# Performance work log

Hardware: AMD Instinct MI355X
Metric: run time of the kernel (lower is better)

Reference implementation:

```python
import jax, jax.numpy as jnp
import numpy as np

B, S, D, H = 2, 2048, 512, 8
HD = D // H
DFF = 4 * D
EPS_LN = 1e-5
EPS_ATTN = 1e-8


def layernorm(x, w, b):
    mu = jnp.mean(x, axis=-1, keepdims=True)
    var = jnp.var(x, axis=-1, keepdims=True)
    return (x - mu) * jax.lax.rsqrt(var + EPS_LN) * w + b


def masked_attention(q_src, v_src, wq, bq, wk, bk, wv, bv, wo, bo, M):
    # q_src/v_src: (B,S,D); M: (B,S,S)
    Bs, Ss, _ = q_src.shape
    Q = (q_src @ wq + bq).reshape(Bs, Ss, H, HD)
    K = (q_src @ wk + bk).reshape(Bs, Ss, H, HD)
    V = (v_src @ wv + bv).reshape(Bs, Ss, H, HD)
    scale = HD ** -0.5
    scores = jnp.einsum('bqhd,bkhd->bhqk', Q, K) * scale
    Mh = M[:, None, :, :]                      # (B,1,S,S) broadcast over heads
    scores = scores * Mh
    A = jax.nn.softmax(scores, axis=-1)
    A = A * Mh                                 # re-mask post-softmax
    A = A / (jnp.sum(jnp.abs(A), axis=-1, keepdims=True) + EPS_ATTN)  # L1 renorm
    out = jnp.einsum('bhqk,bkhd->bqhd', A, V).reshape(Bs, Ss, D)
    return out @ wo + bo


def ffn(x, w1, b1, w2, b2):
    h = jax.nn.gelu(x @ w1 + b1, approximate=False)
    return x + (h @ w2 + b2)                   # FeedForward(num_layers=2) includes residual


def setup_inputs() -> dict:
    key = jax.random.key(0)
    ks = iter(jax.random.split(key, 64))
    nrm = lambda shape, s=0.02: jax.random.normal(next(ks), shape, jnp.float32) * s
    d = {
        'gene_emb': jax.random.normal(next(ks), (B, S, D), jnp.float32),
        'expr_emb': jax.random.normal(next(ks), (B, S, D), jnp.float32),
        'M': jax.random.uniform(next(ks), (B, S, S), jnp.float32),
    }
    # gene attention params (weights stored (in,out))
    for p in ['g_wq', 'g_wk', 'g_wv', 'g_wo']:
        d[p] = nrm((D, D))
    for p in ['g_bq', 'g_bk', 'g_bv', 'g_bo']:
        d[p] = jnp.zeros((D,), jnp.float32)
    # expr attention params (fused proj 2D->D)
    d['e_wf'] = nrm((2 * D, D)); d['e_bf'] = jnp.zeros((D,), jnp.float32)
    for p in ['e_wq', 'e_wk', 'e_wv', 'e_wo']:
        d[p] = nrm((D, D))
    for p in ['e_bq', 'e_bk', 'e_bv', 'e_bo']:
        d[p] = jnp.zeros((D,), jnp.float32)
    # layernorms
    for p in ['ln_g1_w', 'ln_g2_w', 'ln_e1_w', 'ln_e2_w']:
        d[p] = jnp.ones((D,), jnp.float32)
    for p in ['ln_g1_b', 'ln_g2_b', 'ln_e1_b', 'ln_e2_b']:
        d[p] = jnp.zeros((D,), jnp.float32)
    # FFNs
    d['fg_w1'] = nrm((D, DFF)); d['fg_b1'] = jnp.zeros((DFF,), jnp.float32)
    d['fg_w2'] = nrm((DFF, D)); d['fg_b2'] = jnp.zeros((D,), jnp.float32)
    d['fe_w1'] = nrm((D, DFF)); d['fe_b1'] = jnp.zeros((DFF,), jnp.float32)
    d['fe_w2'] = nrm((DFF, D)); d['fe_b2'] = jnp.zeros((D,), jnp.float32)
    return d


def reference(gene_emb, expr_emb, M,
              g_wq, g_bq, g_wk, g_bk, g_wv, g_bv, g_wo, g_bo,
              e_wf, e_bf, e_wq, e_bq, e_wk, e_bk, e_wv, e_bv, e_wo, e_bo,
              ln_g1_w, ln_g1_b, ln_g2_w, ln_g2_b,
              ln_e1_w, ln_e1_b, ln_e2_w, ln_e2_b,
              fg_w1, fg_b1, fg_w2, fg_b2,
              fe_w1, fe_b1, fe_w2, fe_b2):
    # ----- gene branch -----
    xg = layernorm(gene_emb, ln_g1_w, ln_g1_b)
    attn_g = masked_attention(xg, xg, g_wq, g_bq, g_wk, g_bk, g_wv, g_bv, g_wo, g_bo, M)
    x = gene_emb + attn_g
    x_ln = layernorm(x, ln_g2_w, ln_g2_b)
    out_gene = x + ffn(x_ln, fg_w1, fg_b1, fg_w2, fg_b2)
    # ----- expression branch -----
    y_n = layernorm(expr_emb, ln_e1_w, ln_e1_b)
    fused = jnp.concatenate([gene_emb, y_n], axis=-1) @ e_wf + e_bf
    attn_e = masked_attention(fused, y_n, e_wq, e_bq, e_wk, e_bk, e_wv, e_bv, e_wo, e_bo, M)
    y = expr_emb + attn_e
    y_ln = layernorm(y, ln_e2_w, ln_e2_b)
    out_expr = y + ffn(y_ln, fe_w1, fe_b1, fe_w2, fe_b2)
    return (out_gene, out_expr)
```

## Files before the change

### kernel.cpp

```cpp
#include <hip/hip_runtime.h>
#include <math.h>

#define S_LEN 2048
#define DMODEL 512
#define NROWS 4096
#define NHEAD 8
#define HDIM 64
#define LOG2E 1.4426950408889634f

typedef __attribute__((ext_vector_type(8))) __bf16 bf16x8;
typedef __attribute__((ext_vector_type(4))) float f32x4;

__device__ inline float bf2f(unsigned short h) {
    unsigned u = ((unsigned)h) << 16;
    return __builtin_bit_cast(float, u);
}
__device__ inline unsigned short f2bf(float f) {
    unsigned u = __builtin_bit_cast(unsigned, f);
    return (unsigned short)((u + 0x7fffu + ((u >> 16) & 1u)) >> 16);
}

__device__ inline void gl_lds16(const unsigned short* g, unsigned short* l) {
    __builtin_amdgcn_global_load_lds(
        (const __attribute__((address_space(1))) void*)g,
        (__attribute__((address_space(3))) void*)l, 16, 0, 0);
}

__global__ __launch_bounds__(256) void wcast_t(
    const float* __restrict__ W, unsigned short* __restrict__ Wt, int K, int Mo)
{
    __shared__ float t[32][33];
    const int bx = blockIdx.x * 32;
    const int by = blockIdx.y * 32;
    const int tx = threadIdx.x & 31, ty = threadIdx.x >> 5;
    #pragma unroll
    for (int r = 0; r < 4; ++r)
        t[ty + 8 * r][tx] = W[(size_t)(by + ty + 8 * r) * Mo + bx + tx];
    __syncthreads();
    #pragma unroll
    for (int r = 0; r < 4; ++r)
        Wt[(size_t)(bx + ty + 8 * r) * K + by + tx] = f2bf(t[tx][ty + 8 * r]);
}

__global__ __launch_bounds__(256) void wcast_sq8(
    const float* w0, const float* w1, const float* w2, const float* w3,
    const float* w4, const float* w5, const float* w6, const float* w7,
    unsigned short* __restrict__ dst)
{
    const float* srcs[8] = {w0, w1, w2, w3, w4, w5, w6, w7};
    const float* __restrict__ W = srcs[blockIdx.z];
    unsigned short* __restrict__ Wt = dst + (size_t)blockIdx.z * 512 * 512;
    __shared__ float t[32][33];
    const int bx = blockIdx.x * 32, by = blockIdx.y * 32;
    const int tx = threadIdx.x & 31, ty = threadIdx.x >> 5;
    #pragma unroll
    for (int r = 0; r < 4; ++r)
        t[ty + 8 * r][tx] = W[(size_t)(by + ty + 8 * r) * 512 + bx + tx];
    __syncthreads();
    #pragma unroll
    for (int r = 0; r < 4; ++r)
        Wt[(size_t)(bx + ty + 8 * r) * 512 + by + tx] = f2bf(t[tx][ty + 8 * r]);
}

__global__ __launch_bounds__(256) void wcast_t2(
    const float* wA, const float* wB, unsigned short* __restrict__ dst,
    int K, int Mo)
{
    const float* __restrict__ W = blockIdx.z ? wB : wA;
    unsigned short* __restrict__ Wt = dst + (size_t)blockIdx.z * K * Mo;
    __shared__ float t[32][33];
    const int bx = blockIdx.x * 32, by = blockIdx.y * 32;
    const int tx = threadIdx.x & 31, ty = threadIdx.x >> 5;
    #pragma unroll
    for (int r = 0; r < 4; ++r)
        t[ty + 8 * r][tx] = W[(size_t)(by + ty + 8 * r) * Mo + bx + tx];
    __syncthreads();
    #pragma unroll
    for (int r = 0; r < 4; ++r)
        Wt[(size_t)(bx + ty + 8 * r) * K + by + tx] = f2bf(t[tx][ty + 8 * r]);
}

__global__ __launch_bounds__(256) void pack_bias(
    const float* __restrict__ b1, const float* __restrict__ b2,
    const float* __restrict__ b3, float* __restrict__ dst, int n)
{
    int t = blockIdx.x * 256 + threadIdx.x;
    if (t >= n) return;
    float v = (t < 512) ? b1[t] : (t < 1024) ? b2[t - 512] : b3[t - 1024];
    dst[t] = v;
}

__global__ __launch_bounds__(256) void ln_kernel(
    const float* __restrict__ x, const float* __restrict__ w,
    const float* __restrict__ b, unsigned short* __restrict__ y, int ostride)
{
    __shared__ float red[8];
    const int row = blockIdx.x;
    const float* xr = x + (size_t)row * DMODEL;
    const int t = threadIdx.x;
    float v0 = xr[t];
    float v1 = xr[t + 256];
    float s  = v0 + v1;
    float sq = v0 * v0 + v1 * v1;
    #pragma unroll
    for (int o = 32; o > 0; o >>= 1) {
        s  += __shfl_down(s, o);
        sq += __shfl_down(sq, o);
    }
    int wid = t >> 6, lane = t & 63;
    if (lane == 0) { red[wid] = s; red[4 + wid] = sq; }
    __syncthreads();
    float mean = (red[0] + red[1] + red[2] + red[3]) * (1.0f / 512.0f);
    float msq  = (red[4] + red[5] + red[6] + red[7]) * (1.0f / 512.0f);
    float var  = msq - mean * mean;
    float rs   = rsqrtf(var + 1e-5f);
    y[(size_t)row * ostride + t]       = f2bf((v0 - mean) * rs * w[t] + b[t]);
    y[(size_t)row * ostride + t + 256] = f2bf((v1 - mean) * rs * w[t + 256] + b[t + 256]);
}

__global__ __launch_bounds__(256) void ln_cat_kernel(
    const float* __restrict__ xg, const float* __restrict__ xe,
    const float* __restrict__ w, const float* __restrict__ b,
    unsigned short* __restrict__ y)
{
    __shared__ float red[8];
    const int row = blockIdx.x;
    const int t = threadIdx.x;
    const float* gr = xg + (size_t)row * DMODEL;
    const float* er = xe + (size_t)row * DMODEL;
    float g0 = gr[t], g1 = gr[t + 256];
    float v0 = er[t], v1 = er[t + 256];
    float s  = v0 + v1;
    float sq = v0 * v0 + v1 * v1;
    #pragma unroll
    for (int o = 32; o > 0; o >>= 1) {
        s  += __shfl_down(s, o);
        sq += __shfl_down(sq, o);
    }
    int wid = t >> 6, lane = t & 63;
    if (lane == 0) { red[wid] = s; red[4 + wid] = sq; }
    __syncthreads();
    float mean = (red[0] + red[1] + red[2] + red[3]) * (1.0f / 512.0f);
    float msq  = (red[4] + red[5] + red[6] + red[7]) * (1.0f / 512.0f);
    float var  = msq - mean * mean;
    float rs   = rsqrtf(var + 1e-5f);
    unsigned short* yr = y + (size_t)row * 1024;
    yr[t]             = f2bf(g0);
    yr[t + 256]       = f2bf(g1);
    yr[512 + t]       = f2bf((v0 - mean) * rs * w[t] + b[t]);
    yr[512 + t + 256] = f2bf((v1 - mean) * rs * w[t + 256] + b[t + 256]);
}

__global__ __launch_bounds__(256) void vtrans(
    const unsigned short* __restrict__ V, int ldv, unsigned short* __restrict__ Vt)
{
    __shared__ unsigned short t[64][72];
    const int s0 = blockIdx.x * 64, h = blockIdx.y, b = blockIdx.z;
    const int tid = threadIdx.x;
    {
        const int r = tid >> 2, c = (tid & 3) * 16;
        const unsigned short* src = V + (size_t)(b * S_LEN + s0 + r) * ldv + h * 64 + c;
        *(int4*)&t[r][c]     = *(const int4*)(src);
        *(int4*)&t[r][c + 8] = *(const int4*)(src + 8);
    }
    __syncthreads();
    {
        const int d = tid >> 2, s = (tid & 3) * 16;
        unsigned short* dst = Vt + ((size_t)((b * 8 + h) * 64 + d)) * S_LEN + s0 + s;
        unsigned short tmp[16];
        #pragma unroll
        for (int e = 0; e < 16; ++e) tmp[e] = t[s + e][d];
        *(int4*)dst       = *(int4*)&tmp[0];
        *(int4*)(dst + 8) = *(int4*)&tmp[8];
    }
}

__global__ __launch_bounds__(256) void gemm_mfma(
    const unsigned short* __restrict__ A, int lda,
    const unsigned short* __restrict__ Bt,
    const float* __restrict__ bias,
    const float* __restrict__ R1,
    const unsigned short* __restrict__ R2,
    float* __restrict__ Cf, unsigned short* __restrict__ Cb,
    int K, int Mo, int dogelu)
{
    __shared__ __align__(16) unsigned short As[3][128 * 32];
    __shared__ __align__(16) unsigned short Bs[3][128 * 32];
    const int tid = threadIdx.x;
    const int wave = tid >> 6, lane = tid & 63;
    const int wr = wave >> 1, wc = wave & 1;
    const int row0 = blockIdx.y * 128, col0 = blockIdx.x * 128;
    const int l15 = lane & 15, q = lane >> 4;

    f32x4 acc[4][4];
    const f32x4 zz = {0.f, 0.f, 0.f, 0.f};
    #pragma unroll
    for (int i = 0; i < 4; ++i)
        #pragma unroll
        for (int j = 0; j < 4; ++j) acc[i][j] = zz;

    const int nk = K >> 5;
    auto stage = [&](int t, int buf) {
        const int k0 = t * 32;
        #pragma unroll
        for (int r = 0; r < 2; ++r) {
            int idx = r * 256 + tid;
            int row = idx >> 2, kc = idx & 3;
            gl_lds16(&A[(size_t)(row0 + row) * lda + k0 + kc * 8],
                     &As[buf][(size_t)(r * 256 + wave * 64) * 8]);
            gl_lds16(&Bt[(size_t)(col0 + row) * K + k0 + kc * 8],
                     &Bs[buf][(size_t)(r * 256 + wave * 64) * 8]);
        }
    };
    stage(0, 0);
    if (nk > 1) stage(1, 1);

    int cur = 0, nx2 = 2;
    for (int t = 0; t < nk; ++t) {
        if (t + 1 < nk) asm volatile("s_waitcnt vmcnt(4)" ::: "memory");
        else            asm volatile("s_waitcnt vmcnt(0)" ::: "memory");
        __builtin_amdgcn_s_barrier();
        if (t + 2 < nk) stage(t + 2, nx2);

        bf16x8 af[4], bfr[4];
        #pragma unroll
        for (int fi = 0; fi < 4; ++fi)
            af[fi] = *(const bf16x8*)&As[cur][(wr * 64 + fi * 16 + l15) * 32 + q * 8];
        #pragma unroll
        for (int fj = 0; fj < 4; ++fj)
            bfr[fj] = *(const bf16x8*)&Bs[cur][(wc * 64 + fj * 16 + l15) * 32 + q * 8];
        #pragma unroll
        for (int fi = 0; fi < 4; ++fi)
            #pragma unroll
            for (int fj = 0; fj < 4; ++fj)
                acc[fi][fj] = __builtin_amdgcn_mfma_f32_16x16x32_bf16(
                    af[fi], bfr[fj], acc[fi][fj], 0, 0, 0);

        cur = (cur == 2) ? 0 : cur + 1;
        nx2 = (nx2 == 2) ? 0 : nx2 + 1;
    }

    #pragma unroll
    for (int fi = 0; fi < 4; ++fi) {
        #pragma unroll
        for (int reg = 0; reg < 4; ++reg) {
            int row = row0 + wr * 64 + fi * 16 + q * 4 + reg;
            #pragma unroll
            for (int fj = 0; fj < 4; ++fj) {
                int col = col0 + wc * 64 + fj * 16 + l15;
                float v = acc[fi][fj][reg] + bias[col];
                if (dogelu) v = 0.5f * v * (1.0f + erff(v * 0.70710678118654752f));
                size_t off = (size_t)row * Mo + col;
                if (R1) v += R1[off];
                if (R2) v += bf2f(R2[off]);
                if (Cb) Cb[off] = f2bf(v);
                else    Cf[off] = v;
            }
        }
    }
}

__global__ __launch_bounds__(256) void gemm_mfma64(
    const unsigned short* __restrict__ A, int lda,
    const unsigned short* __restrict__ Bt,
    const float* __restrict__ bias,
    const float* __restrict__ R1,
    const unsigned short* __restrict__ R2,
    float* __restrict__ Cf, unsigned short* __restrict__ Cb,
    int K, int Mo, int dogelu)
{
    __shared__ __align__(16) unsigned short As[3][64 * 64];
    __shared__ __align__(16) unsigned short Bs[3][64 * 64];
    const int tid = threadIdx.x;
    const int wave = tid >> 6, lane = tid & 63;
    const int row0 = blockIdx.y * 64, col0 = blockIdx.x * 64;
    const int l15 = lane & 15, q = lane >> 4;

    f32x4 acc[4];
    const f32x4 zz = {0.f, 0.f, 0.f, 0.f};
    #pragma unroll
    for (int j = 0; j < 4; ++j) acc[j] = zz;

    const int nk = K >> 6;
    auto stage = [&](int t, int buf) {
        const int k0 = t * 64;
        #pragma unroll
        for (int r = 0; r < 2; ++r) {
            int idx = r * 256 + tid;
            int row = idx >> 3;
            int kc  = (idx & 7) ^ (row & 7);
            gl_lds16(&A[(size_t)(row0 + row) * lda + k0 + kc * 8],
                     &As[buf][(size_t)(r * 256 + wave * 64) * 8]);
            gl_lds16(&Bt[(size_t)(col0 + row) * K + k0 + kc * 8],
                     &Bs[buf][(size_t)(r * 256 + wave * 64) * 8]);
        }
    };
    stage(0, 0);
    if (nk > 1) stage(1, 1);

    int cur = 0, nx2 = 2;
    for (int t = 0; t < nk; ++t) {
        if (t + 1 < nk) asm volatile("s_waitcnt vmcnt(4)" ::: "memory");
        else            asm volatile("s_waitcnt vmcnt(0)" ::: "memory");
        __builtin_amdgcn_s_barrier();
        if (t + 2 < nk) stage(t + 2, nx2);

        #pragma unroll
        for (int ks = 0; ks < 2; ++ks) {
            const int cx = ((ks * 4 + q) ^ (l15 & 7)) * 8;
            bf16x8 af = *(const bf16x8*)&As[cur][(wave * 16 + l15) * 64 + cx];
            bf16x8 bfr[4];
            #pragma unroll
            for (int fj = 0; fj < 4; ++fj)
                bfr[fj] = *(const bf16x8*)&Bs[cur][(fj * 16 + l15) * 64 + cx];
            #pragma unroll
            for (int fj = 0; fj < 4; ++fj)
                acc[fj] = __builtin_amdgcn_mfma_f32_16x16x32_bf16(af, bfr[fj], acc[fj], 0, 0, 0);
        }

        cur = (cur == 2) ? 0 : cur + 1;
        nx2 = (nx2 == 2) ? 0 : nx2 + 1;
    }

    #pragma unroll
    for (int reg = 0; reg < 4; ++reg) {
        int row = row0 + wave * 16 + q * 4 + reg;
        #pragma unroll
        for (int fj = 0; fj < 4; ++fj) {
            int col = col0 + fj * 16 + l15;
            float v = acc[fj][reg] + bias[col];
            if (dogelu) v = 0.5f * v * (1.0f + erff(v * 0.70710678118654752f));
            size_t off = (size_t)row * Mo + col;
            if (R1) v += R1[off];
            if (R2) v += bf2f(R2[off]);
            if (Cb) Cb[off] = f2bf(v);
            else    Cf[off] = v;
        }
    }
}

__global__ __launch_bounds__(256, 4) void attn_mfma_split(
    const unsigned short* __restrict__ Q, int ldq,
    const unsigned short* __restrict__ Kp, int ldk,
    const unsigned short* __restrict__ Vt,
    const float* __restrict__ M,
    unsigned short* __restrict__ Opart,
    float* __restrict__ stats)
{
    __shared__ __align__(16) unsigned short Ks[64 * 72];
    __shared__ __align__(16) unsigned short Vs[64 * 72];
    __shared__ __align__(16) unsigned short Ps_all[4][16 * 72];

    const int bh = blockIdx.y, b = bh >> 3, h = bh & 7;
    const int q0 = blockIdx.x * 64;
    const int p = blockIdx.z;
    const int tid = threadIdx.x, wave = tid >> 6, lane = tid & 63;
    const int l15 = lane & 15, quad = lane >> 4;
    const int iRow = q0 + wave * 16 + l15;
    const int kBeg = p * (S_LEN / 2), kEnd = kBeg + (S_LEN / 2);

    unsigned short* Ps = &Ps_all[wave][0];

    bf16x8 qf[2];
    {
        const unsigned short* qp = Q + (size_t)(b * S_LEN + iRow) * ldq + h * HDIM + quad * 8;
        #pragma unroll
        for (int ks = 0; ks < 2; ++ks) {
            union { bf16x8 v; unsigned short u[8]; } tq;
            tq.v = *(const bf16x8*)(qp + ks * 32);
            #pragma unroll
            for (int e = 0; e < 8; ++e)
                tq.u[e] = f2bf(bf2f(tq.u[e]) * (0.125f * LOG2E));
            qf[ks] = tq.v;
        }
    }

    const int srow = tid >> 3;
    const int scol = (tid & 7) * 8;
    const unsigned short* kg = Kp + ((size_t)b * S_LEN) * ldk + h * HDIM + scol;
    const unsigned short* vg = Vt + ((size_t)bh * 64 + srow) * S_LEN + scol;
    const float* mrow = M + ((size_t)b * S_LEN + iRow) * S_LEN + quad * 4;

    float rm = -INFINITY, rZ = 0.f, rZm = 0.f;
    f32x4 oacc[4];
    const f32x4 zz = {0.f, 0.f, 0.f, 0.f};
    #pragma unroll
    for (int dt = 0; dt < 4; ++dt) oacc[dt] = zz;

    int4 kv0 = *(const int4*)(kg + (size_t)(kBeg + srow) * ldk);
    int4 kv1 = *(const int4*)(kg + (size_t)(kBeg + srow + 32) * ldk);
    int4 vv0 = *(const int4*)(vg + kBeg);
    int4 vv1 = *(const int4*)(vg + 32 * S_LEN + kBeg);
    *(int4*)&Ks[srow * 72 + scol]        = kv0;
    *(int4*)&Ks[(srow + 32) * 72 + scol] = kv1;
    *(int4*)&Vs[srow * 72 + scol]        = vv0;
    *(int4*)&Vs[(srow + 32) * 72 + scol] = vv1;
    __syncthreads();

    for (int k0 = kBeg; k0 < kEnd; k0 += 64) {
        const bool more = (k0 + 64 < kEnd);
        if (more) {
            kv0 = *(const int4*)(kg + (size_t)(k0 + 64 + srow) * ldk);
            kv1 = *(const int4*)(kg + (size_t)(k0 + 64 + srow + 32) * ldk);
            vv0 = *(const int4*)(vg + k0 + 64);
            vv1 = *(const int4*)(vg + 32 * S_LEN + k0 + 64);
        }
        float4 m4[4];
        #pragma unroll
        for (int jt = 0; jt < 4; ++jt)
            m4[jt] = *(const float4*)(mrow + k0 + jt * 16);

        f32x4 sacc[4];
        #pragma unroll
        for (int jt = 0; jt < 4; ++jt) sacc[jt] = zz;
        __builtin_amdgcn_s_setprio(1);
        #pragma unroll
        for (int jt = 0; jt < 4; ++jt) {
            bf16x8 kf0 = *(const bf16x8*)&Ks[(jt * 16 + l15) * 72 + quad * 8];
            bf16x8 kf1 = *(const bf16x8*)&Ks[(jt * 16 + l15) * 72 + 32 + quad * 8];
            sacc[jt] = __builtin_amdgcn_mfma_f32_16x16x32_bf16(kf0, qf[0], sacc[jt], 0, 0, 0);
            sacc[jt] = __builtin_amdgcn_mfma_f32_16x16x32_bf16(kf1, qf[1], sacc[jt], 0, 0, 0);
        }
        __builtin_amdgcn_s_setprio(0);

        float mxj[4];
        #pragma unroll
        for (int jt = 0; jt < 4; ++jt) {
            float mm[4] = {m4[jt].x, m4[jt].y, m4[jt].z, m4[jt].w};
            #pragma unroll
            for (int r = 0; r < 4; ++r)
                sacc[jt][r] = sacc[jt][r] * mm[r];
            mxj[jt] = fmaxf(fmaxf(sacc[jt][0], sacc[jt][1]),
                            fmaxf(sacc[jt][2], sacc[jt][3]));
        }
        float mx = fmaxf(fmaxf(mxj[0], mxj[1]), fmaxf(mxj[2], mxj[3]));
        mx = fmaxf(mx, __shfl_xor(mx, 16));
        mx = fmaxf(mx, __shfl_xor(mx, 32));
        if (!__all(mx <= rm + 8.0f)) {
            float mn = fmaxf(rm, mx);
            float al = __builtin_amdgcn_exp2f(rm - mn);
            rm = mn; rZ *= al; rZm *= al;
            #pragma unroll
            for (int dt = 0; dt < 4; ++dt)
                #pragma unroll
                for (int r = 0; r < 4; ++r) oacc[dt][r] *= al;
        }

        float z = 0.f, zm = 0.f;
        #pragma unroll
        for (int jt = 0; jt < 4; ++jt) {
            float mm[4] = {m4[jt].x, m4[jt].y, m4[jt].z, m4[jt].w};
            float pv[4];
            #pragma unroll
            for (int r = 0; r < 4; ++r) {
                float e = __builtin_amdgcn_exp2f(sacc[jt][r] - rm);
                float pm = e * mm[r];
                z += e; zm += pm; pv[r] = pm;
            }
            unsigned lo, hi;
            asm("v_cvt_pk_bf16_f32 %0, %1, %2" : "=v"(lo) : "v"(pv[0]), "v"(pv[1]));
            asm("v_cvt_pk_bf16_f32 %0, %1, %2" : "=v"(hi) : "v"(pv[2]), "v"(pv[3]));
            uint2 pk; pk.x = lo; pk.y = hi;
            *(uint2*)&Ps[l15 * 72 + jt * 16 + quad * 4] = pk;
        }
        rZ += z; rZm += zm;

        bf16x8 pf0 = *(const bf16x8*)&Ps[l15 * 72 + quad * 8];
        bf16x8 pf1 = *(const bf16x8*)&Ps[l15 * 72 + 32 + quad * 8];
        __builtin_amdgcn_s_setprio(1);
        #pragma unroll
        for (int dt = 0; dt < 4; ++dt) {
            bf16x8 vf0 = *(const bf16x8*)&Vs[(dt * 16 + l15) * 72 + quad * 8];
            bf16x8 vf1 = *(const bf16x8*)&Vs[(dt * 16 + l15) * 72 + 32 + quad * 8];
            oacc[dt] = __builtin_amdgcn_mfma_f32_16x16x32_bf16(vf0, pf0, oacc[dt], 0, 0, 0);
            oacc[dt] = __builtin_amdgcn_mfma_f32_16x16x32_bf16(vf1, pf1, oacc[dt], 0, 0, 0);
        }
        __builtin_amdgcn_s_setprio(0);

        if (more) {
            __syncthreads();
            *(int4*)&Ks[srow * 72 + scol]        = kv0;
            *(int4*)&Ks[(srow + 32) * 72 + scol] = kv1;
            *(int4*)&Vs[srow * 72 + scol]        = vv0;
            *(int4*)&Vs[(srow + 32) * 72 + scol] = vv1;
            __syncthreads();
        }
    }

    rZ  += __shfl_xor(rZ, 16);  rZ  += __shfl_xor(rZ, 32);
    rZm += __shfl_xor(rZm, 16); rZm += __shfl_xor(rZm, 32);

    unsigned short* op = Opart + (((size_t)(p * 16 + bh) * S_LEN + iRow) * 64);
    #pragma unroll
    for (int dt = 0; dt < 4; ++dt) {
        unsigned lo, hi;
        asm("v_cvt_pk_bf16_f32 %0, %1, %2" : "=v"(lo) : "v"(oacc[dt][0]), "v"(oacc[dt][1]));
        asm("v_cvt_pk_bf16_f32 %0, %1, %2" : "=v"(hi) : "v"(oacc[dt][2]), "v"(oacc[dt][3]));
        uint2 o2; o2.x = lo; o2.y = hi;
        *(uint2*)(op + dt * 16 + quad * 4) = o2;
    }
    if (quad == 0) {
        float4 st; st.x = rm; st.y = rZ; st.z = rZm; st.w = 0.f;
        *(float4*)&stats[(((size_t)p * 16 + bh) * S_LEN + iRow) * 4] = st;
    }
}

__global__ __launch_bounds__(256) void attn_combine(
    const unsigned short* __restrict__ Opart, const float* __restrict__ stats,
    unsigned short* __restrict__ O)
{
    const int bh = blockIdx.y, b = bh >> 3, h = bh & 7;
    const int q0 = blockIdx.x * 64;
    const int tid = threadIdx.x;
    const int i = tid >> 2, dq = (tid & 3) * 16;
    const int qg = q0 + i;

    float4 s0 = *(const float4*)&stats[(((size_t)0 * 16 + bh) * S_LEN + qg) * 4];
    float4 s1 = *(const float4*)&stats[(((size_t)1 * 16 + bh) * S_LEN + qg) * 4];
    float ms = fmaxf(s0.x, s1.x);
    float w0 = __builtin_amdgcn_exp2f(s0.x - ms), w1 = __builtin_amdgcn_exp2f(s1.x - ms);
    float Z  = w0 * s0.y + w1 * s1.y;
    float Zm = w0 * s0.z + w1 * s1.z;
    float inv = 1.0f / (Zm + 1e-8f * Z);
    w0 *= inv; w1 *= inv;

    const unsigned short* p0 = Opart + (((size_t)0 * 16 + bh) * S_LEN + qg) * 64 + dq;
    const unsigned short* p1 = Opart + (((size_t)1 * 16 + bh) * S_LEN + qg) * 64 + dq;
    union { int4 v; unsigned short u[8]; } a0, a1, r;
    unsigned short* dst = O + (size_t)(b * S_LEN + qg) * DMODEL + h * HDIM + dq;
    #pragma unroll
    for (int half = 0; half < 2; ++half) {
        a0.v = *(const int4*)(p0 + half * 8);
        a1.v = *(const int4*)(p1 + half * 8);
        #pragma unroll
        for (int e = 0; e < 8; ++e)
            r.u[e] = f2bf(w0 * bf2f(a0.u[e]) + w1 * bf2f(a1.u[e]));
        *(int4*)(dst + half * 8) = r.v;
    }
}

extern "C" void kernel_launch(void* const* d_in, const int* in_sizes, int n_in,
                              void* d_out, int out_size, void* d_ws, size_t ws_size,
                              hipStream_t stream)
{
    const float* gene_emb = (const float*)d_in[0];
    const float* expr_emb = (const float*)d_in[1];
    const float* M        = (const float*)d_in[2];
    const float* g_wq = (const float*)d_in[3];
    const float* g_wk = (const float*)d_in[4];
    const float* g_wv = (const float*)d_in[5];
    const float* g_wo = (const float*)d_in[6];
    const float* g_bq = (const float*)d_in[7];
    const float* g_bk = (const float*)d_in[8];
    const float* g_bv = (const float*)d_in[9];
    const float* g_bo = (const float*)d_in[10];
    const float* e_wf = (const float*)d_in[11];
    const float* e_bf = (const float*)d_in[12];
    const float* e_wq = (const float*)d_in[13];
    const float* e_wk = (const float*)d_in[14];
    const float* e_wv = (const float*)d_in[15];
    const float* e_wo = (const float*)d_in[16];
    const float* e_bq = (const float*)d_in[17];
    const float* e_bk = (const float*)d_in[18];
    const float* e_bv = (const float*)d_in[19];
    const float* e_bo = (const float*)d_in[20];
    const float* ln_g1_w = (const float*)d_in[21];
    const float* ln_g2_w = (const float*)d_in[22];
    const float* ln_e1_w = (const float*)d_in[23];
    const float* ln_e2_w = (const float*)d_in[24];
    const float* ln_g1_b = (const float*)d_in[25];
    const float* ln_g2_b = (const float*)d_in[26];
    const float* ln_e1_b = (const float*)d_in[27];
    const float* ln_e2_b = (const float*)d_in[28];
    const float* fg_w1 = (const float*)d_in[29];
    const float* fg_b1 = (const float*)d_in[30];
    const float* fg_w2 = (const float*)d_in[31];
    const float* fg_b2 = (const float*)d_in[32];
    const float* fe_w1 = (const float*)d_in[33];
    const float* fe_b1 = (const float*)d_in[34];
    const float* fe_w2 = (const float*)d_in[35];
    const float* fe_b2 = (const float*)d_in[36];

    float* out_gene = (float*)d_out;
    float* out_expr = out_gene + (size_t)NROWS * DMODEL;

    char* ws = (char*)d_ws;
    const size_t MB1 = 1024 * 1024;
    unsigned short* bufA16  = (unsigned short*)(ws + 0 * MB1);
    unsigned short* bufAt16 = (unsigned short*)(ws + 4 * MB1);
    unsigned short* bufQKV  = (unsigned short*)(ws + 8 * MB1);
    unsigned short* bufQKe  = (unsigned short*)(ws + 8 * MB1);
    unsigned short* bufV16  = (unsigned short*)(ws + 16 * MB1);
    unsigned short* bufVt   = (unsigned short*)(ws + 20 * MB1);
    unsigned short* bufCat  = (unsigned short*)(ws + 24 * MB1);
    unsigned short* bufOp   = (unsigned short*)(ws + 24 * MB1);
    float*          bufSt   = (float*)(ws + 32 * MB1);
    float*          bufX    = (float*)(ws + 33 * MB1);
    unsigned short* bufH16  = (unsigned short*)(ws + 8 * MB1);
    char* wp = ws + 41 * MB1;
    unsigned short* sq8    = (unsigned short*)wp;
    unsigned short* gwq_t  = sq8 + 0 * 512 * 512;
    unsigned short* gwk_t  = sq8 + 1 * 512 * 512;
    unsigned short* gwv_t  = sq8 + 2 * 512 * 512;
    unsigned short* gwo_t  = sq8 + 3 * 512 * 512;
    unsigned short* ewq_t  = sq8 + 4 * 512 * 512;
    unsigned short* ewk_t  = sq8 + 5 * 512 * 512;
    unsigned short* ewv_t  = sq8 + 6 * 512 * 512;
    unsigned short* ewo_t  = sq8 + 7 * 512 * 512;
    unsigned short* ewf_t  = sq8 + 8 * 512 * 512;
    unsigned short* ffn1   = ewf_t + 1024 * 512;
    unsigned short* fgw1_t = ffn1;
    unsigned short* few1_t = ffn1 + 512 * 2048;
    unsigned short* ffn2   = few1_t + 512 * 2048;
    unsigned short* fgw2_t = ffn2;
    unsigned short* few2_t = ffn2 + 2048 * 512;
    float* biasg = (float*)(few2_t + 2048 * 512);
    float* biase = biasg + 1536;

    dim3 blk(256);
    dim3 ln_grid(NROWS);
    dim3 g512s(8, 64);
    dim3 g1024(8, 32);
    dim3 g1536(12, 32);
    dim3 g2048(16, 32);
    dim3 attn_grid(S_LEN / 64, 16, 2);
    dim3 comb_grid(S_LEN / 64, 16);
    dim3 vt_grid(S_LEN / 64, NHEAD, 2);

    wcast_sq8<<<dim3(16, 16, 8), blk, 0, stream>>>(
        g_wq, g_wk, g_wv, g_wo, e_wq, e_wk, e_wv, e_wo, sq8);
    wcast_t<<<dim3(16, 32), blk, 0, stream>>>(e_wf, ewf_t, 1024, 512);
    wcast_t2<<<dim3(64, 16, 2), blk, 0, stream>>>(fg_w1, fe_w1, ffn1, 512, 2048);
    wcast_t2<<<dim3(16, 64, 2), blk, 0, stream>>>(fg_w2, fe_w2, ffn2, 2048, 512);
    pack_bias<<<dim3(6), blk, 0, stream>>>(g_bq, g_bk, g_bv, biasg, 1536);
    pack_bias<<<dim3(4), blk, 0, stream>>>(e_bq, e_bk, e_bk, biase, 1024);

    ln_kernel<<<ln_grid, blk, 0, stream>>>(gene_emb, ln_g1_w, ln_g1_b, bufA16, 512);
    gemm_mfma<<<g1536, blk, 0, stream>>>(bufA16, 512, gwq_t, biasg, nullptr, nullptr, nullptr, bufQKV, 512, 1536, 0);
    vtrans<<<vt_grid, blk, 0, stream>>>(bufQKV + 1024, 1536, bufVt);
    attn_mfma_split<<<attn_grid, blk, 0, stream>>>(bufQKV, 1536, bufQKV + 512, 1536, bufVt, M, bufOp, bufSt);
    attn_combine<<<comb_grid, blk, 0, stream>>>(bufOp, bufSt, bufAt16);
    gemm_mfma64<<<g512s, blk, 0, stream>>>(bufAt16, 512, gwo_t, g_bo, gene_emb, nullptr, bufX, nullptr, 512, 512, 0);
    ln_kernel<<<ln_grid, blk, 0, stream>>>(bufX, ln_g2_w, ln_g2_b, bufA16, 512);
    gemm_mfma<<<g2048, blk, 0, stream>>>(bufA16, 512, fgw1_t, fg_b1, nullptr, nullptr, nullptr, bufH16, 512, 2048, 1);
    gemm_mfma64<<<g512s, blk, 0, stream>>>(bufH16, 2048, fgw2_t, fg_b2, bufX, bufA16, out_gene, nullptr, 2048, 512, 0);

    ln_cat_kernel<<<ln_grid, blk, 0, stream>>>(gene_emb, expr_emb, ln_e1_w, ln_e1_b, bufCat);
    gemm_mfma64<<<g512s, blk, 0, stream>>>(bufCat, 1024, ewf_t, e_bf, nullptr, nullptr, nullptr, bufA16, 1024, 512, 0);
    gemm_mfma<<<g1024, blk, 0, stream>>>(bufA16, 512, ewq_t, biase, nullptr, nullptr, nullptr, bufQKe, 512, 1024, 0);
    gemm_mfma64<<<g512s, blk, 0, stream>>>(bufCat + 512, 1024, ewv_t, e_bv, nullptr, nullptr, nullptr, bufV16, 512, 512, 0);
    vtrans<<<vt_grid, blk, 0, stream>>>(bufV16, 512, bufVt);
    attn_mfma_split<<<attn_grid, blk, 0, stream>>>(bufQKe, 1024, bufQKe + 512, 1024, bufVt, M, bufOp, bufSt);
    attn_combine<<<comb_grid, blk, 0, stream>>>(bufOp, bufSt, bufAt16);
    gemm_mfma64<<<g512s, blk, 0, stream>>>(bufAt16, 512, ewo_t, e_bo, expr_emb, nullptr, bufX, nullptr, 512, 512, 0);
    ln_kernel<<<ln_grid, blk, 0, stream>>>(bufX, ln_e2_w, ln_e2_b, bufA16, 512);
    gemm_mfma<<<g2048, blk, 0, stream>>>(bufA16, 512, few1_t, fe_b1, nullptr, nullptr, nullptr, bufH16, 512, 2048, 1);
    gemm_mfma64<<<g512s, blk, 0, stream>>>(bufH16, 2048, few2_t, fe_b2, bufX, bufA16, out_expr, nullptr, 2048, 512, 0);
}
```

Measured before the change: 520.8 us.

## Merge prep kernels, fuse front layernorms, drop attention KV split

All weight-cast, transpose and bias-pack launches are merged into one prep_all kernel. The two front layernorms become a single ln_front kernel that also writes the concatenated buffer. The two-way KV-split attention plus its combine kernel is replaced by one attention kernel per query tile that normalises in place, and the mask rows are now prefetched one tile ahead. This cuts launch count and the partial-output round trip, but halves the attention grid (512 blocks), so the GPU has less parallelism to work with.

Result: no change. 521.2 us (+0.1%).

```diff
diff --git a/kernel.cpp b/kernel.cpp
--- a/kernel.cpp
+++ b/kernel.cpp
@@ -26,68 +26,101 @@
         (__attribute__((address_space(3))) void*)l, 16, 0, 0);
 }
 
-__global__ __launch_bounds__(256) void wcast_t(
-    const float* __restrict__ W, unsigned short* __restrict__ Wt, int K, int Mo)
-{
-    __shared__ float t[32][33];
-    const int bx = blockIdx.x * 32;
-    const int by = blockIdx.y * 32;
-    const int tx = threadIdx.x & 31, ty = threadIdx.x >> 5;
+__global__ __launch_bounds__(256) void prep_all(
+    const float* g_wq, const float* g_wk, const float* g_wv, const float* g_wo,
+    const float* e_wq, const float* e_wk, const float* e_wv, const float* e_wo,
+    const float* e_wf, const float* fg_w1, const float* fe_w1,
+    const float* fg_w2, const float* fe_w2,
+    const float* g_bq, const float* g_bk, const float* g_bv,
+    const float* e_bq, const float* e_bk,
+    unsigned short* __restrict__ wbase, float* __restrict__ biasg,
+    float* __restrict__ biase)
+{
+    const int id = blockIdx.x;
+    const int tid = threadIdx.x;
+    if (id >= 6656) {
+        int t = id - 6656;
+        if (t < 6) {
+            int i = t * 256 + tid;
+            biasg[i] = (i < 512) ? g_bq[i] : (i < 1024) ? g_bk[i - 512] : g_bv[i - 1024];
+        } else {
+            int i = (t - 6) * 256 + tid;
+            biase[i] = (i < 512) ? e_bq[i] : e_bk[i - 512];
+        }
+        return;
+    }
+    const float* W; unsigned short* Wt; int K, Mo, bx, by;
+    if (id < 2048) {
+        const float* srcs[8] = {g_wq, g_wk, g_wv, g_wo, e_wq, e_wk, e_wv, e_wo};
+        int m = id >> 8, t = id & 255;
+        W = srcs[m]; Wt = wbase + (size_t)m * 512 * 512; K = 512; Mo = 512;
+        bx = (t & 15) * 32; by = (t >> 4) * 32;
+    } else if (id < 2560) {
+        int t = id - 2048;
+        W = e_wf; Wt = wbase + 8 * 512 * 512; K = 1024; Mo = 512;
+        bx = (t & 15) * 32; by = (t >> 4) * 32;
+    } else if (id < 4608) {
+        int t = id - 2560; int which = t >> 10; t &= 1023;
+        W = which ? fe_w1 : fg_w1;
+        Wt = wbase + 8 * 512 * 512 + 1024 * 512 + (size_t)which * 512 * 2048;
+        K = 512; Mo = 2048;
+        bx = (t & 63) * 32; by = (t >> 6) * 32;
+    } else {
+        int t = id - 4608; int which = t >> 10; t &= 1023;
+        W = which ? fe_w2 : fg_w2;
+        Wt = wbase + 8 * 512 * 512 + 1024 * 512 + 2 * 512 * 2048 + (size_t)which * 2048 * 512;
+        K = 2048; Mo = 512;
+        bx = (t & 15) * 32; by = (t >> 4) * 32;
+    }
+    __shared__ float tsh[32][33];
+    const int tx = tid & 31, ty = tid >> 5;
     #pragma unroll
     for (int r = 0; r < 4; ++r)
-        t[ty + 8 * r][tx] = W[(size_t)(by + ty + 8 * r) * Mo + bx + tx];
+        tsh[ty + 8 * r][tx] = W[(size_t)(by + ty + 8 * r) * Mo + bx + tx];
     __syncthreads();
     #pragma unroll
     for (int r = 0; r < 4; ++r)
-        Wt[(size_t)(bx + ty + 8 * r) * K + by + tx] = f2bf(t[tx][ty + 8 * r]);
-}
-
-__global__ __launch_bounds__(256) void wcast_sq8(
-    const float* w0, const float* w1, const float* w2, const float* w3,
-    const float* w4, const float* w5, const float* w6, const float* w7,
-    unsigned short* __restrict__ dst)
-{
-    const float* srcs[8] = {w0, w1, w2, w3, w4, w5, w6, w7};
-    const float* __restrict__ W = srcs[blockIdx.z];
-    unsigned short* __restrict__ Wt = dst + (size_t)blockIdx.z * 512 * 512;
-    __shared__ float t[32][33];
-    const int bx = blockIdx.x * 32, by = blockIdx.y * 32;
-    const int tx = threadIdx.x & 31, ty = threadIdx.x >> 5;
-    #pragma unroll
-    for (int r = 0; r < 4; ++r)
-        t[ty + 8 * r][tx] = W[(size_t)(by + ty + 8 * r) * 512 + bx + tx];
+        Wt[(size_t)(bx + ty + 8 * r) * K + by + tx] = f2bf(tsh[tx][ty + 8 * r]);
+}
+
+__global__ __launch_bounds__(256) void ln_front(
+    const float* __restrict__ gene, const float* __restrict__ expr,
+    const float* __restrict__ gw, const float* __restrict__ gb,
+    const float* __restrict__ ew, const float* __restrict__ eb,
+    unsigned short* __restrict__ yg,
+    unsigned short* __restrict__ ycat)
+{
+    __shared__ float red[16];
+    const int row = blockIdx.x, t = threadIdx.x;
+    const float* gr = gene + (size_t)row * DMODEL;
+    const float* er = expr + (size_t)row * DMODEL;
+    float g0 = gr[t], g1 = gr[t + 256];
+    float e0 = er[t], e1 = er[t + 256];
+    float sg = g0 + g1, sqg = g0 * g0 + g1 * g1;
+    float se = e0 + e1, sqe = e0 * e0 + e1 * e1;
+    #pragma unroll
+    for (int o = 32; o > 0; o >>= 1) {
+        sg += __shfl_down(sg, o);  sqg += __shfl_down(sqg, o);
+        se += __shfl_down(se, o);  sqe += __shfl_down(sqe, o);
+    }
+    int wid = t >> 6, lane = t & 63;
+    if (lane == 0) {
+        red[wid] = sg; red[4 + wid] = sqg; red[8 + wid] = se; red[12 + wid] = sqe;
+    }
     __syncthreads();
-    #pragma unroll
-    for (int r = 0; r < 4; ++r)
-        Wt[(size_t)(bx + ty + 8 * r) * 512 + by + tx] = f2bf(t[tx][ty + 8 * r]);
-}
-
-__global__ __launch_bounds__(256) void wcast_t2(
-    const float* wA, const float* wB, unsigned short* __restrict__ dst,
-    int K, int Mo)
-{
-    const float* __restrict__ W = blockIdx.z ? wB : wA;
-    unsigned short* __restrict__ Wt = dst + (size_t)blockIdx.z * K * Mo;
-    __shared__ float t[32][33];
-    const int bx = blockIdx.x * 32, by = blockIdx.y * 32;
-    const int tx = threadIdx.x & 31, ty = threadIdx.x >> 5;
-    #pragma unroll
-    for (int r = 0; r < 4; ++r)
-        t[ty + 8 * r][tx] = W[(size_t)(by + ty + 8 * r) * Mo + bx + tx];
-    __syncthreads();
-    #pragma unroll
-    for (int r = 0; r < 4; ++r)
-        Wt[(size_t)(bx + ty + 8 * r) * K + by + tx] = f2bf(t[tx][ty + 8 * r]);
-}
-
-__global__ __launch_bounds__(256) void pack_bias(
-    const float* __restrict__ b1, const float* __restrict__ b2,
-    const float* __restrict__ b3, float* __restrict__ dst, int n)
-{
-    int t = blockIdx.x * 256 + threadIdx.x;
-    if (t >= n) return;
-    float v = (t < 512) ? b1[t] : (t < 1024) ? b2[t - 512] : b3[t - 1024];
-    dst[t] = v;
+    float mg  = (red[0] + red[1] + red[2] + red[3]) * (1.0f / 512.0f);
+    float qg_ = (red[4] + red[5] + red[6] + red[7]) * (1.0f / 512.0f);
+    float me  = (red[8] + red[9] + red[10] + red[11]) * (1.0f / 512.0f);
+    float qe_ = (red[12] + red[13] + red[14] + red[15]) * (1.0f / 512.0f);
+    float rg = rsqrtf(qg_ - mg * mg + 1e-5f);
+    float re = rsqrtf(qe_ - me * me + 1e-5f);
+    yg[(size_t)row * 512 + t]         = f2bf((g0 - mg) * rg * gw[t] + gb[t]);
+    yg[(size_t)row * 512 + t + 256]   = f2bf((g1 - mg) * rg * gw[t + 256] + gb[t + 256]);
+    unsigned short* yr = ycat + (size_t)row * 1024;
+    yr[t]             = f2bf(g0);
+    yr[t + 256]       = f2bf(g1);
+    yr[512 + t]       = f2bf((e0 - me) * re * ew[t] + eb[t]);
+    yr[512 + t + 256] = f2bf((e1 - me) * re * ew[t + 256] + eb[t + 256]);
 }
 
 __global__ __launch_bounds__(256) void ln_kernel(
@@ -116,39 +149,6 @@
     float rs   = rsqrtf(var + 1e-5f);
     y[(size_t)row * ostride + t]       = f2bf((v0 - mean) * rs * w[t] + b[t]);
     y[(size_t)row * ostride + t + 256] = f2bf((v1 - mean) * rs * w[t + 256] + b[t + 256]);
-}
-
-__global__ __launch_bounds__(256) void ln_cat_kernel(
-    const float* __restrict__ xg, const float* __restrict__ xe,
-    const float* __restrict__ w, const float* __restrict__ b,
-    unsigned short* __restrict__ y)
-{
-    __shared__ float red[8];
-    const int row = blockIdx.x;
-    const int t = threadIdx.x;
-    const float* gr = xg + (size_t)row * DMODEL;
-    const float* er = xe + (size_t)row * DMODEL;
-    float g0 = gr[t], g1 = gr[t + 256];
-    float v0 = er[t], v1 = er[t + 256];
-    float s  = v0 + v1;
-    float sq = v0 * v0 + v1 * v1;
-    #pragma unroll
-    for (int o = 32; o > 0; o >>= 1) {
-        s  += __shfl_down(s, o);
-        sq += __shfl_down(sq, o);
-    }
-    int wid = t >> 6, lane = t & 63;
-    if (lane == 0) { red[wid] = s; red[4 + wid] = sq; }
-    __syncthreads();
-    float mean = (red[0] + red[1] + red[2] + red[3]) * (1.0f / 512.0f);
-    float msq  = (red[4] + red[5] + red[6] + red[7]) * (1.0f / 512.0f);
-    float var  = msq - mean * mean;
-    float rs   = rsqrtf(var + 1e-5f);
-    unsigned short* yr = y + (size_t)row * 1024;
-    yr[t]             = f2bf(g0);
-    yr[t + 256]       = f2bf(g1);
-    yr[512 + t]       = f2bf((v0 - mean) * rs * w[t] + b[t]);
-    yr[512 + t + 256] = f2bf((v1 - mean) * rs * w[t + 256] + b[t + 256]);
 }
 
 __global__ __launch_bounds__(256) void vtrans(
@@ -339,13 +339,12 @@
     }
 }
 
-__global__ __launch_bounds__(256, 4) void attn_mfma_split(
+__global__ __launch_bounds__(256, 4) void attn_mfma(
     const unsigned short* __restrict__ Q, int ldq,
     const unsigned short* __restrict__ Kp, int ldk,
     const unsigned short* __restrict__ Vt,
     const float* __restrict__ M,
-    unsigned short* __restrict__ Opart,
-    float* __restrict__ stats)
+    unsigned short* __restrict__ O)
 {
     __shared__ __align__(16) unsigned short Ks[64 * 72];
     __shared__ __align__(16) unsigned short Vs[64 * 72];
@@ -353,11 +352,9 @@
 
     const int bh = blockIdx.y, b = bh >> 3, h = bh & 7;
     const int q0 = blockIdx.x * 64;
-    const int p = blockIdx.z;
     const int tid = threadIdx.x, wave = tid >> 6, lane = tid & 63;
     const int l15 = lane & 15, quad = lane >> 4;
     const int iRow = q0 + wave * 16 + l15;
-    const int kBeg = p * (S_LEN / 2), kEnd = kBeg + (S_LEN / 2);
 
     unsigned short* Ps = &Ps_all[wave][0];
 
@@ -387,28 +384,31 @@
     #pragma unroll
     for (int dt = 0; dt < 4; ++dt) oacc[dt] = zz;
 
-    int4 kv0 = *(const int4*)(kg + (size_t)(kBeg + srow) * ldk);
-    int4 kv1 = *(const int4*)(kg + (size_t)(kBeg + srow + 32) * ldk);
-    int4 vv0 = *(const int4*)(vg + kBeg);
-    int4 vv1 = *(const int4*)(vg + 32 * S_LEN + kBeg);
+    int4 kv0 = *(const int4*)(kg + (size_t)srow * ldk);
+    int4 kv1 = *(const int4*)(kg + (size_t)(srow + 32) * ldk);
+    int4 vv0 = *(const int4*)(vg);
+    int4 vv1 = *(const int4*)(vg + 32 * S_LEN);
+    float4 m4[4], m4n[4];
+    #pragma unroll
+    for (int jt = 0; jt < 4; ++jt)
+        m4[jt] = *(const float4*)(mrow + jt * 16);
     *(int4*)&Ks[srow * 72 + scol]        = kv0;
     *(int4*)&Ks[(srow + 32) * 72 + scol] = kv1;
     *(int4*)&Vs[srow * 72 + scol]        = vv0;
     *(int4*)&Vs[(srow + 32) * 72 + scol] = vv1;
     __syncthreads();
 
-    for (int k0 = kBeg; k0 < kEnd; k0 += 64) {
-        const bool more = (k0 + 64 < kEnd);
+    for (int k0 = 0; k0 < S_LEN; k0 += 64) {
+        const bool more = (k0 + 64 < S_LEN);
         if (more) {
             kv0 = *(const int4*)(kg + (size_t)(k0 + 64 + srow) * ldk);
             kv1 = *(const int4*)(kg + (size_t)(k0 + 64 + srow + 32) * ldk);
             vv0 = *(const int4*)(vg + k0 + 64);
             vv1 = *(const int4*)(vg + 32 * S_LEN + k0 + 64);
-        }
-        float4 m4[4];
-        #pragma unroll
-        for (int jt = 0; jt < 4; ++jt)
-            m4[jt] = *(const float4*)(mrow + k0 + jt * 16);
+            #pragma unroll
+            for (int jt = 0; jt < 4; ++jt)
+                m4n[jt] = *(const float4*)(mrow + k0 + 64 + jt * 16);
+        }
 
         f32x4 sacc[4];
         #pragma unroll
@@ -484,58 +484,25 @@
             *(int4*)&Vs[srow * 72 + scol]        = vv0;
             *(int4*)&Vs[(srow + 32) * 72 + scol] = vv1;
             __syncthreads();
+            #pragma unroll
+            for (int jt = 0; jt < 4; ++jt) m4[jt] = m4n[jt];
         }
     }
 
     rZ  += __shfl_xor(rZ, 16);  rZ  += __shfl_xor(rZ, 32);
     rZm += __shfl_xor(rZm, 16); rZm += __shfl_xor(rZm, 32);
-
-    unsigned short* op = Opart + (((size_t)(p * 16 + bh) * S_LEN + iRow) * 64);
+    float inv = 1.0f / (rZm + 1e-8f * rZ);
+
+    unsigned short* op = O + (size_t)(b * S_LEN + iRow) * DMODEL + h * HDIM;
     #pragma unroll
     for (int dt = 0; dt < 4; ++dt) {
+        float o0 = oacc[dt][0] * inv, o1 = oacc[dt][1] * inv;
+        float o2 = oacc[dt][2] * inv, o3 = oacc[dt][3] * inv;
         unsigned lo, hi;
-        asm("v_cvt_pk_bf16_f32 %0, %1, %2" : "=v"(lo) : "v"(oacc[dt][0]), "v"(oacc[dt][1]));
-        asm("v_cvt_pk_bf16_f32 %0, %1, %2" : "=v"(hi) : "v"(oacc[dt][2]), "v"(oacc[dt][3]));
-        uint2 o2; o2.x = lo; o2.y = hi;
-        *(uint2*)(op + dt * 16 + quad * 4) = o2;
-    }
-    if (quad == 0) {
-        float4 st; st.x = rm; st.y = rZ; st.z = rZm; st.w = 0.f;
-        *(float4*)&stats[(((size_t)p * 16 + bh) * S_LEN + iRow) * 4] = st;
-    }
-}
-
-__global__ __launch_bounds__(256) void attn_combine(
-    const unsigned short* __restrict__ Opart, const float* __restrict__ stats,
-    unsigned short* __restrict__ O)
-{
-    const int bh = blockIdx.y, b = bh >> 3, h = bh & 7;
-    const int q0 = blockIdx.x * 64;
-    const int tid = threadIdx.x;
-    const int i = tid >> 2, dq = (tid & 3) * 16;
-    const int qg = q0 + i;
-
-    float4 s0 = *(const float4*)&stats[(((size_t)0 * 16 + bh) * S_LEN + qg) * 4];
-    float4 s1 = *(const float4*)&stats[(((size_t)1 * 16 + bh) * S_LEN + qg) * 4];
-    float ms = fmaxf(s0.x, s1.x);
-    float w0 = __builtin_amdgcn_exp2f(s0.x - ms), w1 = __builtin_amdgcn_exp2f(s1.x - ms);
-    float Z  = w0 * s0.y + w1 * s1.y;
-    float Zm = w0 * s0.z + w1 * s1.z;
-    float inv = 1.0f / (Zm + 1e-8f * Z);
-    w0 *= inv; w1 *= inv;
-
-    const unsigned short* p0 = Opart + (((size_t)0 * 16 + bh) * S_LEN + qg) * 64 + dq;
-    const unsigned short* p1 = Opart + (((size_t)1 * 16 + bh) * S_LEN + qg) * 64 + dq;
-    union { int4 v; unsigned short u[8]; } a0, a1, r;
-    unsigned short* dst = O + (size_t)(b * S_LEN + qg) * DMODEL + h * HDIM + dq;
-    #pragma unroll
-    for (int half = 0; half < 2; ++half) {
-        a0.v = *(const int4*)(p0 + half * 8);
-        a1.v = *(const int4*)(p1 + half * 8);
-        #pragma unroll
-        for (int e = 0; e < 8; ++e)
-            r.u[e] = f2bf(w0 * bf2f(a0.u[e]) + w1 * bf2f(a1.u[e]));
-        *(int4*)(dst + half * 8) = r.v;
+        asm("v_cvt_pk_bf16_f32 %0, %1, %2" : "=v"(lo) : "v"(o0), "v"(o1));
+        asm("v_cvt_pk_bf16_f32 %0, %1, %2" : "=v"(hi) : "v"(o2), "v"(o3));
+        uint2 o2v; o2v.x = lo; o2v.y = hi;
+        *(uint2*)(op + dt * 16 + quad * 4) = o2v;
     }
 }
 
@@ -593,18 +560,13 @@
     unsigned short* bufV16  = (unsigned short*)(ws + 16 * MB1);
     unsigned short* bufVt   = (unsigned short*)(ws + 20 * MB1);
     unsigned short* bufCat  = (unsigned short*)(ws + 24 * MB1);
-    unsigned short* bufOp   = (unsigned short*)(ws + 24 * MB1);
-    float*          bufSt   = (float*)(ws + 32 * MB1);
     float*          bufX    = (float*)(ws + 33 * MB1);
     unsigned short* bufH16  = (unsigned short*)(ws + 8 * MB1);
     char* wp = ws + 41 * MB1;
     unsigned short* sq8    = (unsigned short*)wp;
     unsigned short* gwq_t  = sq8 + 0 * 512 * 512;
-    unsigned short* gwk_t  = sq8 + 1 * 512 * 512;
-    unsigned short* gwv_t  = sq8 + 2 * 512 * 512;
     unsigned short* gwo_t  = sq8 + 3 * 512 * 512;
     unsigned short* ewq_t  = sq8 + 4 * 512 * 512;
-    unsigned short* ewk_t  = sq8 + 5 * 512 * 512;
     unsigned short* ewv_t  = sq8 + 6 * 512 * 512;
     unsigned short* ewo_t  = sq8 + 7 * 512 * 512;
     unsigned short* ewf_t  = sq8 + 8 * 512 * 512;
@@ -623,35 +585,31 @@
     dim3 g1024(8, 32);
     dim3 g1536(12, 32);
     dim3 g2048(16, 32);
-    dim3 attn_grid(S_LEN / 64, 16, 2);
-    dim3 comb_grid(S_LEN / 64, 16);
+    dim3 attn_grid(S_LEN / 64, 16);
     dim3 vt_grid(S_LEN / 64, NHEAD, 2);
 
-    wcast_sq8<<<dim3(16, 16, 8), blk, 0, stream>>>(
-        g_wq, g_wk, g_wv, g_wo, e_wq, e_wk, e_wv, e_wo, sq8);
-    wcast_t<<<dim3(16, 32), blk, 0, stream>>>(e_wf, ewf_t, 1024, 512);
-    wcast_t2<<<dim3(64, 16, 2), blk, 0, stream>>>(fg_w1, fe_w1, ffn1, 512, 2048);
-    wcast_t2<<<dim3(16, 64, 2), blk, 0, stream>>>(fg_w2, fe_w2, ffn2, 2048, 512);
-    pack_bias<<<dim3(6), blk, 0, stream>>>(g_bq, g_bk, g_bv, biasg, 1536);
-    pack_bias<<<dim3(4), blk, 0, stream>>>(e_bq, e_bk, e_bk, biase, 1024);
-
-    ln_kernel<<<ln_grid, blk, 0, stream>>>(gene_emb, ln_g1_w, ln_g1_b, bufA16, 512);
+    prep_all<<<dim3(6666), blk, 0, stream>>>(
+        g_wq, g_wk, g_wv, g_wo, e_wq, e_wk, e_wv, e_wo,
+        e_wf, fg_w1, fe_w1, fg_w2, fe_w2,
+        g_bq, g_bk, g_bv, e_bq, e_bk,
+        sq8, biasg, biase);
+
+    ln_front<<<ln_grid, blk, 0, stream>>>(
+        gene_emb, expr_emb, ln_g1_w, ln_g1_b, ln_e1_w, ln_e1_b, bufA16, bufCat);
+
     gemm_mfma<<<g1536, blk, 0, stream>>>(bufA16, 512, gwq_t, biasg, nullptr, nullptr, nullptr, bufQKV, 512, 1536, 0);
     vtrans<<<vt_grid, blk, 0, stream>>>(bufQKV + 1024, 1536, bufVt);
-    attn_mfma_split<<<attn_grid, blk, 0, stream>>>(bufQKV, 1536, bufQKV + 512, 1536, bufVt, M, bufOp, bufSt);
-    attn_combine<<<comb_grid, blk, 0, stream>>>(bufOp, bufSt, bufAt16);
+    attn_mfma<<<attn_grid, blk, 0, stream>>>(bufQKV, 1536, bufQKV + 512, 1536, bufVt, M, bufAt16);
     gemm_mfma64<<<g512s, blk, 0, stream>>>(bufAt16, 512, gwo_t, g_bo, gene_emb, nullptr, bufX, nullptr, 512, 512, 0);
     ln_kernel<<<ln_grid, blk, 0, stream>>>(bufX, ln_g2_w, ln_g2_b, bufA16, 512);
     gemm_mfma<<<g2048, blk, 0, stream>>>(bufA16, 512, fgw1_t, fg_b1, nullptr, nullptr, nullptr, bufH16, 512, 2048, 1);
     gemm_mfma64<<<g512s, blk, 0, stream>>>(bufH16, 2048, fgw2_t, fg_b2, bufX, bufA16, out_gene, nullptr, 2048, 512, 0);
 
-    ln_cat_kernel<<<ln_grid, blk, 0, stream>>>(gene_emb, expr_emb, ln_e1_w, ln_e1_b, bufCat);
     gemm_mfma64<<<g512s, blk, 0, stream>>>(bufCat, 1024, ewf_t, e_bf, nullptr, nullptr, nullptr, bufA16, 1024, 512, 0);
     gemm_mfma<<<g1024, blk, 0, stream>>>(bufA16, 512, ewq_t, biase, nullptr, nullptr, nullptr, bufQKe, 512, 1024, 0);
     gemm_mfma64<<<g512s, blk, 0, stream>>>(bufCat + 512, 1024, ewv_t, e_bv, nullptr, nullptr, nullptr, bufV16, 512, 512, 0);
     vtrans<<<vt_grid, blk, 0, stream>>>(bufV16, 512, bufVt);
-    attn_mfma_split<<<attn_grid, blk, 0, stream>>>(bufQKe, 1024, bufQKe + 512, 1024, bufVt, M, bufOp, bufSt);
-    attn_combine<<<comb_grid, blk, 0, stream>>>(bufOp, bufSt, bufAt16);
+    attn_mfma<<<attn_grid, blk, 0, stream>>>(bufQKe, 1024, bufQKe + 512, 1024, bufVt, M, bufAt16);
     gemm_mfma64<<<g512s, blk, 0, stream>>>(bufAt16, 512, ewo_t, e_bo, expr_emb, nullptr, bufX, nullptr, 512, 512, 0);
     ln_kernel<<<ln_grid, blk, 0, stream>>>(bufX, ln_e2_w, ln_e2_b, bufA16, 512);
     gemm_mfma<<<g2048, blk, 0, stream>>>(bufA16, 512, few1_t, fe_b1, nullptr, nullptr, nullptr, bufH16, 512, 2048, 1);
```
